# Performance work log

Measured on AMD Instinct MI355X. Metric: run time of the kernel, lower is better.

Reference implementation:

```python
import jax, jax.numpy as jnp
import numpy as np

B, T, M, P = 64, 2048, 512, 512


def setup_inputs() -> dict:
    key = jax.random.key(0)
    ks = jax.random.split(key, 9)
    s = 0.02
    return {
        "hidden_state": jax.random.normal(ks[0], (B, P), jnp.float32),
        "cell_state": jax.random.normal(ks[1], (B, P), jnp.float32),
        "encoder_h": jax.random.normal(ks[2], (B, T, M), jnp.float32),
        # Dense W_d: (2p -> m)
        "W_d": jax.random.normal(ks[3], (2 * P, M), jnp.float32) * s,
        "b_wd": jnp.zeros((M,), jnp.float32),
        # Dense U_d: (m -> m)
        "U_d": jax.random.normal(ks[4], (M, M), jnp.float32) * s,
        "b_ud": jnp.zeros((M,), jnp.float32),
        # Dense v_d: (m -> 1)
        "v_d": jax.random.normal(ks[5], (M, 1), jnp.float32) * s,
        "b_vd": jnp.zeros((1,), jnp.float32),
    }


def reference(hidden_state, cell_state, encoder_h, W_d, b_wd, U_d, b_ud, v_d, b_vd):
    # W_d(RepeatVector(T)(concat([d, s]))): the Dense is applied to the same
    # (B, 2p) vector at every time step, so compute it once and broadcast.
    ds = jnp.concatenate([hidden_state, cell_state], axis=-1)          # (B, 2p)
    ds_proj = ds @ W_d + b_wd                                          # (B, m)
    enc_proj = jnp.einsum('btm,mn->btn', encoder_h, U_d) + b_ud        # (B, T, m)
    e = jnp.tanh(ds_proj[:, None, :] + enc_proj)                       # (B, T, m)
    l = e @ v_d + b_vd                                                 # (B, T, 1)
    return jax.nn.softmax(l, axis=1)                                   # softmax over T
```

## Files before the change

kernel.cpp:

```cpp
#include <hip/hip_runtime.h>
#include <cstdint>
#include <cstddef>


typedef float  floatx4 __attribute__((ext_vector_type(4)));
typedef short  shortx8 __attribute__((ext_vector_type(8)));
typedef unsigned int uintx4 __attribute__((ext_vector_type(4)));

__device__ __forceinline__ short f2bf_rne(float f) {
  unsigned u = __float_as_uint(f);
  unsigned r = u + 0x7FFFu + ((u >> 16) & 1u);
  return (short)(r >> 16);
}

__device__ __forceinline__ unsigned pack_bf_trunc(float lo, float hi) {
  return __builtin_amdgcn_perm(__float_as_uint(hi), __float_as_uint(lo), 0x07060302u);
}

#define GLOAD_LDS16(gptr, lptr)                                                 \
  __builtin_amdgcn_global_load_lds(                                             \
      (const __attribute__((address_space(1))) void*)(gptr),                    \
      (__attribute__((address_space(3))) void*)(lptr), 16, 0, 0)

#define SB() __builtin_amdgcn_sched_barrier(0)
#define WAIT_VM0() asm volatile("s_waitcnt vmcnt(0)" ::: "memory")
#define WAIT_VM4() asm volatile("s_waitcnt vmcnt(4)" ::: "memory")
#define WAIT_VM8() asm volatile("s_waitcnt vmcnt(8)" ::: "memory")
#define WAIT_LGKM0() asm volatile("s_waitcnt lgkmcnt(0)" ::: "memory")
#define BAR() __builtin_amdgcn_s_barrier()

extern "C" __global__ __launch_bounds__(256) void prep_kernel(
    const float* __restrict__ hidden, const float* __restrict__ cell,
    const float* __restrict__ W_d, const float* __restrict__ b_wd,
    const float* __restrict__ U_d, const float* __restrict__ b_ud,
    float* __restrict__ S, short* __restrict__ UT, float* __restrict__ lzero)
{
  int bx = blockIdx.x, tid = threadIdx.x;
  if (bx < 128) {
    int idx = bx * 256 + tid;
    int b = idx >> 9, n = idx & 511;
    const float* h = hidden + b * 512;
    const float* c = cell   + b * 512;
    float a0 = b_wd[n] + b_ud[n], a1 = 0.f, a2 = 0.f, a3 = 0.f;
    for (int k = 0; k < 512; k += 4) {
      a0 = fmaf(h[k + 0], W_d[(k + 0) * 512 + n], a0);
      a1 = fmaf(h[k + 1], W_d[(k + 1) * 512 + n], a1);
      a2 = fmaf(h[k + 2], W_d[(k + 2) * 512 + n], a2);
      a3 = fmaf(h[k + 3], W_d[(k + 3) * 512 + n], a3);
    }
    for (int k = 0; k < 512; k += 4) {
      a0 = fmaf(c[k + 0], W_d[(k + 512) * 512 + n], a0);
      a1 = fmaf(c[k + 1], W_d[(k + 513) * 512 + n], a1);
      a2 = fmaf(c[k + 2], W_d[(k + 514) * 512 + n], a2);
      a3 = fmaf(c[k + 3], W_d[(k + 515) * 512 + n], a3);
    }
    S[idx] = (a0 + a1) + (a2 + a3);
  } else if (bx < 384) {
    int idx  = (bx - 128) * 1024 + tid * 4;
    int tile = idx >> 14;
    int cb = tile >> 3, kt = tile & 7;
    int sI = idx & 16383;
    int n  = sI >> 6;
    int gp = (sI >> 3) & 7;
    int bb = sI & 7;
    int gl = gp ^ (n & 7);
    int k0 = kt * 64 + gl * 8 + bb;
    int ng = cb * 256 + n;
    unsigned lo = (unsigned short)f2bf_rne(U_d[(size_t)(k0 + 0) * 512 + ng]) |
                  ((unsigned)(unsigned short)f2bf_rne(U_d[(size_t)(k0 + 1) * 512 + ng]) << 16);
    unsigned hi = (unsigned short)f2bf_rne(U_d[(size_t)(k0 + 2) * 512 + ng]) |
                  ((unsigned)(unsigned short)f2bf_rne(U_d[(size_t)(k0 + 3) * 512 + ng]) << 16);
    uint2 w; w.x = lo; w.y = hi;
    *(uint2*)(UT + idx) = w;
  } else {
    int idx = ((bx - 384) * 256 + tid) * 4;
    floatx4 z = {0.f, 0.f, 0.f, 0.f};
    *(floatx4*)(lzero + idx) = z;
  }
}

extern "C" __global__ __launch_bounds__(512, 2) void attn_gemm(
    const float* __restrict__ A, const short* __restrict__ UT,
    const float* __restrict__ S, const float* __restrict__ vd,
    float* __restrict__ lout)
{
  __shared__ short As[2][16384];
  __shared__ short Bs[2][16384];

  const int tid = threadIdx.x;
  const int bx  = blockIdx.x;
  const int xcd = bx & 7;
  const int wg  = xcd * 128 + (bx >> 3);
  const int cb  = wg & 1;
  const int rb  = wg >> 1;
  const int row0 = rb << 8;
  const int col0 = cb << 8;
  const int wave = tid >> 6;
  const int lane = tid & 63;
  const int wr = wave >> 2, wc = wave & 3;
  const int q = lane >> 4, l15 = lane & 15;

  const int arow = tid >> 1;
  const int ah   = tid & 1;
  const float* aptr = A + (size_t)(row0 + arow) * 512 + ah * 32;
  const int awbase = arow * 64 + ((((ah * 4) ^ (arow & 7)) & 7) << 3);

  const short* bptr = UT + (size_t)cb * 131072 + (wave * 4) * 512 + lane * 8;
  const int bldsbase = wave * 2048;

  const int fgp = (q ^ (l15 & 7)) << 3;
  const int afrag0 = (wr * 128 + l15) * 64 + fgp;
  const int bfrag0 = (wc * 64  + l15) * 64 + fgp;

  floatx4 acc[8][4];
#pragma unroll
  for (int i = 0; i < 8; ++i)
#pragma unroll
    for (int j = 0; j < 4; ++j)
      acc[i][j] = (floatx4){0.f, 0.f, 0.f, 0.f};

  floatx4 areg[8];

  SB();
#pragma unroll
  for (int i = 0; i < 8; ++i) areg[i] = *(const floatx4*)(aptr + i * 4);
  SB();
#pragma unroll
  for (int j = 0; j < 4; ++j)
    GLOAD_LDS16(bptr + j * 512, &Bs[0][bldsbase + j * 512]);
  SB();
  WAIT_VM4(); SB();
#pragma unroll
  for (int gi = 0; gi < 4; ++gi) {
    uintx4 w;
    w.x = pack_bf_trunc(areg[2 * gi].x, areg[2 * gi].y);
    w.y = pack_bf_trunc(areg[2 * gi].z, areg[2 * gi].w);
    w.z = pack_bf_trunc(areg[2 * gi + 1].x, areg[2 * gi + 1].y);
    w.w = pack_bf_trunc(areg[2 * gi + 1].z, areg[2 * gi + 1].w);
    *(uintx4*)(&As[0][awbase ^ (gi * 8)]) = w;
  }
  SB();
#pragma unroll
  for (int i = 0; i < 8; ++i) areg[i] = *(const floatx4*)(aptr + 64 + i * 4);
  SB();
  WAIT_VM8(); SB();
  WAIT_LGKM0(); SB();
  BAR(); SB();

  shortx8 af[4][2], bfr[4][2];

#pragma unroll 2
  for (int t = 0; t < 8; ++t) {
    const int cur = t & 1;
    const short* Ab = &As[cur][0];
    const short* Bb = &Bs[cur][0];
    short* An = &As[cur ^ 1][0];
    short* Bn = &Bs[cur ^ 1][0];
    const short* bnext = bptr + (t + 1) * 16384;

#pragma unroll
    for (int tc = 0; tc < 2; ++tc)
#pragma unroll
      for (int s = 0; s < 2; ++s)
        bfr[tc][s] = *(const shortx8*)(Bb + ((bfrag0 + tc * 1024) ^ (s * 32)));
#pragma unroll
    for (int tr = 0; tr < 4; ++tr)
#pragma unroll
      for (int s = 0; s < 2; ++s)
        af[tr][s] = *(const shortx8*)(Ab + ((afrag0 + tr * 1024) ^ (s * 32)));
    SB();
    if (t < 7) {
      GLOAD_LDS16(bnext,       Bn + bldsbase);
      GLOAD_LDS16(bnext + 512, Bn + bldsbase + 512);
    }
    SB();
    BAR(); WAIT_LGKM0(); SB();
    __builtin_amdgcn_s_setprio(1);
#pragma unroll
    for (int tr = 0; tr < 4; ++tr)
#pragma unroll
      for (int tc = 0; tc < 2; ++tc)
#pragma unroll
        for (int s = 0; s < 2; ++s)
          acc[tr][tc] = __builtin_amdgcn_mfma_f32_16x16x32_bf16(
              af[tr][s], bfr[tc][s], acc[tr][tc], 0, 0, 0);
    __builtin_amdgcn_s_setprio(0);
    SB(); BAR();

#pragma unroll
    for (int tc = 2; tc < 4; ++tc)
#pragma unroll
      for (int s = 0; s < 2; ++s)
        bfr[tc][s] = *(const shortx8*)(Bb + ((bfrag0 + tc * 1024) ^ (s * 32)));
    SB();
    if (t < 7) {
      GLOAD_LDS16(bnext + 1024, Bn + bldsbase + 1024);
      GLOAD_LDS16(bnext + 1536, Bn + bldsbase + 1536);
    }
    SB();
    BAR(); WAIT_LGKM0(); SB();
    __builtin_amdgcn_s_setprio(1);
#pragma unroll
    for (int tr = 0; tr < 4; ++tr)
#pragma unroll
      for (int tc = 2; tc < 4; ++tc)
#pragma unroll
        for (int s = 0; s < 2; ++s)
          acc[tr][tc] = __builtin_amdgcn_mfma_f32_16x16x32_bf16(
              af[tr][s], bfr[tc][s], acc[tr][tc], 0, 0, 0);
    __builtin_amdgcn_s_setprio(0);
    SB(); BAR();

    if (t < 7) {
      WAIT_VM4(); SB();
#pragma unroll
      for (int gi = 0; gi < 4; ++gi) {
        uintx4 w;
        w.x = pack_bf_trunc(areg[2 * gi].x, areg[2 * gi].y);
        w.y = pack_bf_trunc(areg[2 * gi].z, areg[2 * gi].w);
        w.z = pack_bf_trunc(areg[2 * gi + 1].x, areg[2 * gi + 1].y);
        w.w = pack_bf_trunc(areg[2 * gi + 1].z, areg[2 * gi + 1].w);
        *(uintx4*)(An + (awbase ^ (gi * 8))) = w;
      }
      SB();
    }
#pragma unroll
    for (int tr = 0; tr < 4; ++tr)
#pragma unroll
      for (int s = 0; s < 2; ++s)
        af[tr][s] = *(const shortx8*)(Ab + ((afrag0 + (tr + 4) * 1024) ^ (s * 32)));
    SB();
    if (t < 6) {
#pragma unroll
      for (int i = 0; i < 8; ++i)
        areg[i] = *(const floatx4*)(aptr + (t + 2) * 64 + i * 4);
    }
    SB();
    BAR(); WAIT_LGKM0(); SB();
    __builtin_amdgcn_s_setprio(1);
#pragma unroll
    for (int tr = 0; tr < 4; ++tr)
#pragma unroll
      for (int tc = 0; tc < 2; ++tc)
#pragma unroll
        for (int s = 0; s < 2; ++s)
          acc[tr + 4][tc] = __builtin_amdgcn_mfma_f32_16x16x32_bf16(
              af[tr][s], bfr[tc][s], acc[tr + 4][tc], 0, 0, 0);
    __builtin_amdgcn_s_setprio(0);
    SB(); BAR();

    __builtin_amdgcn_s_setprio(1);
#pragma unroll
    for (int tr = 0; tr < 4; ++tr)
#pragma unroll
      for (int tc = 2; tc < 4; ++tc)
#pragma unroll
        for (int s = 0; s < 2; ++s)
          acc[tr + 4][tc] = __builtin_amdgcn_mfma_f32_16x16x32_bf16(
              af[tr][s], bfr[tc][s], acc[tr + 4][tc], 0, 0, 0);
    __builtin_amdgcn_s_setprio(0);
    SB();
    if (t < 7) {
      if (t < 6) { WAIT_VM8(); }
      else       { WAIT_VM0(); }
      SB();
      BAR(); SB();
    }
  }

  const int bb = rb >> 3;
  const float* Srow = S + bb * 512;
  float sv[4], vv[4];
#pragma unroll
  for (int tc = 0; tc < 4; ++tc) {
    int n = col0 + wc * 64 + tc * 16 + l15;
    sv[tc] = Srow[n];
    vv[tc] = vd[n];
  }
#pragma unroll
  for (int tr = 0; tr < 8; ++tr) {
#pragma unroll
    for (int r = 0; r < 4; ++r) {
      float ssum = 0.f;
#pragma unroll
      for (int tc = 0; tc < 4; ++tc) {
        float x = acc[tr][tc][r] + sv[tc];
        x = fminf(15.f, fmaxf(-15.f, x));
        float e2 = __expf(2.f * x);
        float e = (e2 - 1.f) / (e2 + 1.f);
        ssum += e * vv[tc];
      }
      ssum += __shfl_xor(ssum, 1);
      ssum += __shfl_xor(ssum, 2);
      ssum += __shfl_xor(ssum, 4);
      ssum += __shfl_xor(ssum, 8);
      if (l15 == 0) {
        int row = row0 + wr * 128 + tr * 16 + q * 4 + r;
        atomicAdd(lout + row, ssum);
      }
    }
  }
}

extern "C" __global__ __launch_bounds__(256) void softmax_t(float* __restrict__ l)
{
  int b = blockIdx.x, tid = threadIdx.x;
  int wave = tid >> 6, lane = tid & 63;
  float* row = l + (size_t)b * 2048;
  float v[8];
  float mx = -3.4e38f;
#pragma unroll
  for (int i = 0; i < 8; ++i) { v[i] = row[tid + i * 256]; mx = fmaxf(mx, v[i]); }
#pragma unroll
  for (int m = 1; m < 64; m <<= 1) mx = fmaxf(mx, __shfl_xor(mx, m));
  __shared__ float red[8];
  if (lane == 0) red[wave] = mx;
  __syncthreads();
  mx = fmaxf(fmaxf(red[0], red[1]), fmaxf(red[2], red[3]));
  float s = 0.f;
#pragma unroll
  for (int i = 0; i < 8; ++i) { v[i] = __expf(v[i] - mx); s += v[i]; }
#pragma unroll
  for (int m = 1; m < 64; m <<= 1) s += __shfl_xor(s, m);
  if (lane == 0) red[4 + wave] = s;
  __syncthreads();
  s = red[4] + red[5] + red[6] + red[7];
  float inv = 1.f / s;
#pragma unroll
  for (int i = 0; i < 8; ++i) row[tid + i * 256] = v[i] * inv;
}

extern "C" void kernel_launch(void* const* d_in, const int* in_sizes, int n_in,
                              void* d_out, int out_size, void* d_ws, size_t ws_size,
                              hipStream_t stream) {
  const float* hidden = (const float*)d_in[0];
  const float* cell   = (const float*)d_in[1];
  const float* enc    = (const float*)d_in[2];
  const float* W_d    = (const float*)d_in[3];
  const float* b_wd   = (const float*)d_in[4];
  const float* U_d    = (const float*)d_in[5];
  const float* b_ud   = (const float*)d_in[6];
  const float* v_d    = (const float*)d_in[7];
  float* out = (float*)d_out;
  float* S   = (float*)d_ws;
  short* UT  = (short*)((char*)d_ws + 32768 * sizeof(float));

  hipLaunchKernelGGL(prep_kernel, dim3(512), dim3(256), 0, stream,
                     hidden, cell, W_d, b_wd, U_d, b_ud, S, UT, out);
  hipLaunchKernelGGL(attn_gemm, dim3(1024), dim3(512), 0, stream,
                     enc, UT, S, v_d, out);
  hipLaunchKernelGGL(softmax_t, dim3(64), dim3(256), 0, stream, out);
}
```

Before: 506.7 us.

## Load U_d fragments directly from global into registers, shrink GEMM tile to 128x256

The B operand (bf16 U_d, now stored in plain n-major layout) no longer goes through LDS. Each wave loads its MFMA fragments straight from global or L2 into double-buffered registers. The workgroup tile shrinks from 256x256 with 8 waves to 128x256 with 4 waves, launched as 2048 blocks. The k-loop is fully unrolled through a templated iteration, and LDS use drops to the A double buffer only. This removes the B LDS staging and several barriers per iteration, in exchange for more global and L2 traffic for B and more registers for the prefetched fragments.

Measured after the change: 574.4 us. 13.4% more time.

```diff
diff --git a/kernel.cpp b/kernel.cpp
--- a/kernel.cpp
+++ b/kernel.cpp
@@ -17,14 +17,8 @@
   return __builtin_amdgcn_perm(__float_as_uint(hi), __float_as_uint(lo), 0x07060302u);
 }
 
-#define GLOAD_LDS16(gptr, lptr)                                                 \
-  __builtin_amdgcn_global_load_lds(                                             \
-      (const __attribute__((address_space(1))) void*)(gptr),                    \
-      (__attribute__((address_space(3))) void*)(lptr), 16, 0, 0)
-
 #define SB() __builtin_amdgcn_sched_barrier(0)
 #define WAIT_VM0() asm volatile("s_waitcnt vmcnt(0)" ::: "memory")
-#define WAIT_VM4() asm volatile("s_waitcnt vmcnt(4)" ::: "memory")
 #define WAIT_VM8() asm volatile("s_waitcnt vmcnt(8)" ::: "memory")
 #define WAIT_LGKM0() asm volatile("s_waitcnt lgkmcnt(0)" ::: "memory")
 #define BAR() __builtin_amdgcn_s_barrier()
@@ -56,20 +50,12 @@
     }
     S[idx] = (a0 + a1) + (a2 + a3);
   } else if (bx < 384) {
-    int idx  = (bx - 128) * 1024 + tid * 4;
-    int tile = idx >> 14;
-    int cb = tile >> 3, kt = tile & 7;
-    int sI = idx & 16383;
-    int n  = sI >> 6;
-    int gp = (sI >> 3) & 7;
-    int bb = sI & 7;
-    int gl = gp ^ (n & 7);
-    int k0 = kt * 64 + gl * 8 + bb;
-    int ng = cb * 256 + n;
-    unsigned lo = (unsigned short)f2bf_rne(U_d[(size_t)(k0 + 0) * 512 + ng]) |
-                  ((unsigned)(unsigned short)f2bf_rne(U_d[(size_t)(k0 + 1) * 512 + ng]) << 16);
-    unsigned hi = (unsigned short)f2bf_rne(U_d[(size_t)(k0 + 2) * 512 + ng]) |
-                  ((unsigned)(unsigned short)f2bf_rne(U_d[(size_t)(k0 + 3) * 512 + ng]) << 16);
+    int idx = (bx - 128) * 1024 + tid * 4;
+    int n = idx >> 9, k0 = idx & 511;
+    unsigned lo = (unsigned short)f2bf_rne(U_d[(size_t)(k0 + 0) * 512 + n]) |
+                  ((unsigned)(unsigned short)f2bf_rne(U_d[(size_t)(k0 + 1) * 512 + n]) << 16);
+    unsigned hi = (unsigned short)f2bf_rne(U_d[(size_t)(k0 + 2) * 512 + n]) |
+                  ((unsigned)(unsigned short)f2bf_rne(U_d[(size_t)(k0 + 3) * 512 + n]) << 16);
     uint2 w; w.x = lo; w.y = hi;
     *(uint2*)(UT + idx) = w;
   } else {
@@ -79,38 +65,128 @@
   }
 }
 
-extern "C" __global__ __launch_bounds__(512, 2) void attn_gemm(
+struct GemmState {
+  short (*As)[8192];
+  const float* aptr;
+  const short* bfp[4];
+  int afrag0, awbase;
+};
+
+template <int T>
+__device__ __forceinline__ void kiter(
+    GemmState& st, shortx8 (&bfr)[2][4][2], floatx4 (&areg)[8],
+    floatx4 (&acc)[8][4])
+{
+  constexpr int CUR = T & 1;
+  constexpr int NXT = CUR ^ 1;
+  const short* Ab = &st.As[CUR][0];
+  shortx8 af[4][2];
+
+#pragma unroll
+  for (int tr = 0; tr < 4; ++tr)
+#pragma unroll
+    for (int s = 0; s < 2; ++s)
+      af[tr][s] = *(const shortx8*)(Ab + ((st.afrag0 + tr * 1024) ^ (s * 32)));
+  SB();
+  if constexpr (T < 7) {
+#pragma unroll
+    for (int tc = 0; tc < 4; ++tc)
+#pragma unroll
+      for (int s = 0; s < 2; ++s)
+        bfr[NXT][tc][s] = *(const shortx8*)(st.bfp[tc] + (T + 1) * 64 + s * 32);
+  }
+  SB();
+  WAIT_LGKM0(); SB();
+  __builtin_amdgcn_s_setprio(1);
+#pragma unroll
+  for (int tr = 0; tr < 4; ++tr)
+#pragma unroll
+    for (int tc = 0; tc < 4; ++tc)
+#pragma unroll
+      for (int s = 0; s < 2; ++s)
+        acc[tr][tc] = __builtin_amdgcn_mfma_f32_16x16x32_bf16(
+            af[tr][s], bfr[CUR][tc][s], acc[tr][tc], 0, 0, 0);
+  __builtin_amdgcn_s_setprio(0);
+  SB(); BAR(); SB();
+
+  if constexpr (T < 7) {
+    WAIT_VM8(); SB();
+    short* An = &st.As[NXT][0];
+#pragma unroll
+    for (int gi = 0; gi < 4; ++gi) {
+      uintx4 w;
+      w.x = pack_bf_trunc(areg[2 * gi].x, areg[2 * gi].y);
+      w.y = pack_bf_trunc(areg[2 * gi].z, areg[2 * gi].w);
+      w.z = pack_bf_trunc(areg[2 * gi + 1].x, areg[2 * gi + 1].y);
+      w.w = pack_bf_trunc(areg[2 * gi + 1].z, areg[2 * gi + 1].w);
+      *(uintx4*)(An + (st.awbase ^ (gi * 8))) = w;
+    }
+    SB();
+  }
+#pragma unroll
+  for (int tr = 0; tr < 4; ++tr)
+#pragma unroll
+    for (int s = 0; s < 2; ++s)
+      af[tr][s] = *(const shortx8*)(Ab + ((st.afrag0 + (tr + 4) * 1024) ^ (s * 32)));
+  SB();
+  if constexpr (T < 6) {
+#pragma unroll
+    for (int i = 0; i < 8; ++i)
+      areg[i] = *(const floatx4*)(st.aptr + (T + 2) * 64 + i * 4);
+  }
+  SB();
+  WAIT_LGKM0(); SB();
+  __builtin_amdgcn_s_setprio(1);
+#pragma unroll
+  for (int tr = 0; tr < 4; ++tr)
+#pragma unroll
+    for (int tc = 0; tc < 4; ++tc)
+#pragma unroll
+      for (int s = 0; s < 2; ++s)
+        acc[tr + 4][tc] = __builtin_amdgcn_mfma_f32_16x16x32_bf16(
+            af[tr][s], bfr[CUR][tc][s], acc[tr + 4][tc], 0, 0, 0);
+  __builtin_amdgcn_s_setprio(0);
+  SB();
+  if constexpr (T < 7) {
+    if constexpr (T < 6) { WAIT_VM8(); }
+    else                 { WAIT_VM0(); }
+    SB(); BAR(); SB();
+  }
+}
+
+extern "C" __global__ __launch_bounds__(256, 2) void attn_gemm(
     const float* __restrict__ A, const short* __restrict__ UT,
     const float* __restrict__ S, const float* __restrict__ vd,
     float* __restrict__ lout)
 {
-  __shared__ short As[2][16384];
-  __shared__ short Bs[2][16384];
+  __shared__ short As[2][8192];
 
   const int tid = threadIdx.x;
   const int bx  = blockIdx.x;
   const int xcd = bx & 7;
-  const int wg  = xcd * 128 + (bx >> 3);
+  const int wg  = xcd * 256 + (bx >> 3);
   const int cb  = wg & 1;
   const int rb  = wg >> 1;
-  const int row0 = rb << 8;
+  const int row0 = rb << 7;
   const int col0 = cb << 8;
   const int wave = tid >> 6;
   const int lane = tid & 63;
-  const int wr = wave >> 2, wc = wave & 3;
+  const int wc = wave;
   const int q = lane >> 4, l15 = lane & 15;
+
+  GemmState st;
+  st.As = As;
 
   const int arow = tid >> 1;
   const int ah   = tid & 1;
-  const float* aptr = A + (size_t)(row0 + arow) * 512 + ah * 32;
-  const int awbase = arow * 64 + ((((ah * 4) ^ (arow & 7)) & 7) << 3);
-
-  const short* bptr = UT + (size_t)cb * 131072 + (wave * 4) * 512 + lane * 8;
-  const int bldsbase = wave * 2048;
-
-  const int fgp = (q ^ (l15 & 7)) << 3;
-  const int afrag0 = (wr * 128 + l15) * 64 + fgp;
-  const int bfrag0 = (wc * 64  + l15) * 64 + fgp;
+  st.aptr   = A + (size_t)(row0 + arow) * 512 + ah * 32;
+  st.awbase = arow * 64 + ((((ah * 4) ^ (arow & 7)) & 7) << 3);
+
+#pragma unroll
+  for (int tc = 0; tc < 4; ++tc)
+    st.bfp[tc] = UT + (size_t)(col0 + wc * 64 + tc * 16 + l15) * 512 + q * 8;
+
+  st.afrag0 = l15 * 64 + ((q ^ (l15 & 7)) << 3);
 
   floatx4 acc[8][4];
 #pragma unroll
@@ -120,16 +196,19 @@
       acc[i][j] = (floatx4){0.f, 0.f, 0.f, 0.f};
 
   floatx4 areg[8];
-
-  SB();
-#pragma unroll
-  for (int i = 0; i < 8; ++i) areg[i] = *(const floatx4*)(aptr + i * 4);
-  SB();
-#pragma unroll
-  for (int j = 0; j < 4; ++j)
-    GLOAD_LDS16(bptr + j * 512, &Bs[0][bldsbase + j * 512]);
-  SB();
-  WAIT_VM4(); SB();
+  shortx8 bfr[2][4][2];
+
+  SB();
+#pragma unroll
+  for (int i = 0; i < 8; ++i) areg[i] = *(const floatx4*)(st.aptr + i * 4);
+  SB();
+#pragma unroll
+  for (int tc = 0; tc < 4; ++tc)
+#pragma unroll
+    for (int s = 0; s < 2; ++s)
+      bfr[0][tc][s] = *(const shortx8*)(st.bfp[tc] + s * 32);
+  SB();
+  WAIT_VM8(); SB();
 #pragma unroll
   for (int gi = 0; gi < 4; ++gi) {
     uintx4 w;
@@ -137,138 +216,26 @@
     w.y = pack_bf_trunc(areg[2 * gi].z, areg[2 * gi].w);
     w.z = pack_bf_trunc(areg[2 * gi + 1].x, areg[2 * gi + 1].y);
     w.w = pack_bf_trunc(areg[2 * gi + 1].z, areg[2 * gi + 1].w);
-    *(uintx4*)(&As[0][awbase ^ (gi * 8)]) = w;
-  }
-  SB();
-#pragma unroll
-  for (int i = 0; i < 8; ++i) areg[i] = *(const floatx4*)(aptr + 64 + i * 4);
+    *(uintx4*)(&As[0][st.awbase ^ (gi * 8)]) = w;
+  }
+  SB();
+#pragma unroll
+  for (int i = 0; i < 8; ++i) areg[i] = *(const floatx4*)(st.aptr + 64 + i * 4);
   SB();
   WAIT_VM8(); SB();
   WAIT_LGKM0(); SB();
   BAR(); SB();
 
-  shortx8 af[4][2], bfr[4][2];
-
-#pragma unroll 2
-  for (int t = 0; t < 8; ++t) {
-    const int cur = t & 1;
-    const short* Ab = &As[cur][0];
-    const short* Bb = &Bs[cur][0];
-    short* An = &As[cur ^ 1][0];
-    short* Bn = &Bs[cur ^ 1][0];
-    const short* bnext = bptr + (t + 1) * 16384;
-
-#pragma unroll
-    for (int tc = 0; tc < 2; ++tc)
-#pragma unroll
-      for (int s = 0; s < 2; ++s)
-        bfr[tc][s] = *(const shortx8*)(Bb + ((bfrag0 + tc * 1024) ^ (s * 32)));
-#pragma unroll
-    for (int tr = 0; tr < 4; ++tr)
-#pragma unroll
-      for (int s = 0; s < 2; ++s)
-        af[tr][s] = *(const shortx8*)(Ab + ((afrag0 + tr * 1024) ^ (s * 32)));
-    SB();
-    if (t < 7) {
-      GLOAD_LDS16(bnext,       Bn + bldsbase);
-      GLOAD_LDS16(bnext + 512, Bn + bldsbase + 512);
-    }
-    SB();
-    BAR(); WAIT_LGKM0(); SB();
-    __builtin_amdgcn_s_setprio(1);
-#pragma unroll
-    for (int tr = 0; tr < 4; ++tr)
-#pragma unroll
-      for (int tc = 0; tc < 2; ++tc)
-#pragma unroll
-        for (int s = 0; s < 2; ++s)
-          acc[tr][tc] = __builtin_amdgcn_mfma_f32_16x16x32_bf16(
-              af[tr][s], bfr[tc][s], acc[tr][tc], 0, 0, 0);
-    __builtin_amdgcn_s_setprio(0);
-    SB(); BAR();
-
-#pragma unroll
-    for (int tc = 2; tc < 4; ++tc)
-#pragma unroll
-      for (int s = 0; s < 2; ++s)
-        bfr[tc][s] = *(const shortx8*)(Bb + ((bfrag0 + tc * 1024) ^ (s * 32)));
-    SB();
-    if (t < 7) {
-      GLOAD_LDS16(bnext + 1024, Bn + bldsbase + 1024);
-      GLOAD_LDS16(bnext + 1536, Bn + bldsbase + 1536);
-    }
-    SB();
-    BAR(); WAIT_LGKM0(); SB();
-    __builtin_amdgcn_s_setprio(1);
-#pragma unroll
-    for (int tr = 0; tr < 4; ++tr)
-#pragma unroll
-      for (int tc = 2; tc < 4; ++tc)
-#pragma unroll
-        for (int s = 0; s < 2; ++s)
-          acc[tr][tc] = __builtin_amdgcn_mfma_f32_16x16x32_bf16(
-              af[tr][s], bfr[tc][s], acc[tr][tc], 0, 0, 0);
-    __builtin_amdgcn_s_setprio(0);
-    SB(); BAR();
-
-    if (t < 7) {
-      WAIT_VM4(); SB();
-#pragma unroll
-      for (int gi = 0; gi < 4; ++gi) {
-        uintx4 w;
-        w.x = pack_bf_trunc(areg[2 * gi].x, areg[2 * gi].y);
-        w.y = pack_bf_trunc(areg[2 * gi].z, areg[2 * gi].w);
-        w.z = pack_bf_trunc(areg[2 * gi + 1].x, areg[2 * gi + 1].y);
-        w.w = pack_bf_trunc(areg[2 * gi + 1].z, areg[2 * gi + 1].w);
-        *(uintx4*)(An + (awbase ^ (gi * 8))) = w;
-      }
-      SB();
-    }
-#pragma unroll
-    for (int tr = 0; tr < 4; ++tr)
-#pragma unroll
-      for (int s = 0; s < 2; ++s)
-        af[tr][s] = *(const shortx8*)(Ab + ((afrag0 + (tr + 4) * 1024) ^ (s * 32)));
-    SB();
-    if (t < 6) {
-#pragma unroll
-      for (int i = 0; i < 8; ++i)
-        areg[i] = *(const floatx4*)(aptr + (t + 2) * 64 + i * 4);
-    }
-    SB();
-    BAR(); WAIT_LGKM0(); SB();
-    __builtin_amdgcn_s_setprio(1);
-#pragma unroll
-    for (int tr = 0; tr < 4; ++tr)
-#pragma unroll
-      for (int tc = 0; tc < 2; ++tc)
-#pragma unroll
-        for (int s = 0; s < 2; ++s)
-          acc[tr + 4][tc] = __builtin_amdgcn_mfma_f32_16x16x32_bf16(
-              af[tr][s], bfr[tc][s], acc[tr + 4][tc], 0, 0, 0);
-    __builtin_amdgcn_s_setprio(0);
-    SB(); BAR();
-
-    __builtin_amdgcn_s_setprio(1);
-#pragma unroll
-    for (int tr = 0; tr < 4; ++tr)
-#pragma unroll
-      for (int tc = 2; tc < 4; ++tc)
-#pragma unroll
-        for (int s = 0; s < 2; ++s)
-          acc[tr + 4][tc] = __builtin_amdgcn_mfma_f32_16x16x32_bf16(
-              af[tr][s], bfr[tc][s], acc[tr + 4][tc], 0, 0, 0);
-    __builtin_amdgcn_s_setprio(0);
-    SB();
-    if (t < 7) {
-      if (t < 6) { WAIT_VM8(); }
-      else       { WAIT_VM0(); }
-      SB();
-      BAR(); SB();
-    }
-  }
-
-  const int bb = rb >> 3;
+  kiter<0>(st, bfr, areg, acc);
+  kiter<1>(st, bfr, areg, acc);
+  kiter<2>(st, bfr, areg, acc);
+  kiter<3>(st, bfr, areg, acc);
+  kiter<4>(st, bfr, areg, acc);
+  kiter<5>(st, bfr, areg, acc);
+  kiter<6>(st, bfr, areg, acc);
+  kiter<7>(st, bfr, areg, acc);
+
+  const int bb = rb >> 4;
   const float* Srow = S + bb * 512;
   float sv[4], vv[4];
 #pragma unroll
@@ -295,7 +262,7 @@
       ssum += __shfl_xor(ssum, 4);
       ssum += __shfl_xor(ssum, 8);
       if (l15 == 0) {
-        int row = row0 + wr * 128 + tr * 16 + q * 4 + r;
+        int row = row0 + tr * 16 + q * 4 + r;
         atomicAdd(lout + row, ssum);
       }
     }
@@ -347,7 +314,7 @@
 
   hipLaunchKernelGGL(prep_kernel, dim3(512), dim3(256), 0, stream,
                      hidden, cell, W_d, b_wd, U_d, b_ud, S, UT, out);
-  hipLaunchKernelGGL(attn_gemm, dim3(1024), dim3(512), 0, stream,
+  hipLaunchKernelGGL(attn_gemm, dim3(2048), dim3(256), 0, stream,
                      enc, UT, S, v_d, out);
   hipLaunchKernelGGL(softmax_t, dim3(64), dim3(256), 0, stream, out);
 }
```
